# Optimization experiments

Hardware: AMD Instinct MI355X
Metric: run time of the kernel (lower is better)

## Reference

```python
import jax, jax.numpy as jnp
from jax import lax
import numpy as np

S, D, L, H, C = 128, 3, 16, 512, 10
B, T = 32, 16384


def setup_inputs() -> dict:
    key = jax.random.key(0)
    ks = jax.random.split(key, 6)
    x = jax.random.normal(ks[0], (B, D, T), dtype=jnp.float32)
    shapelets = jax.random.normal(ks[1], (S, 1, D, L), dtype=jnp.float32)  # OIHW, one per shapelet
    W1 = jax.random.normal(ks[2], (H, S), dtype=jnp.float32) * (1.0 / np.sqrt(S))
    b1 = jnp.zeros((H,), dtype=jnp.float32)
    W2 = jax.random.normal(ks[3], (C, H), dtype=jnp.float32) * (1.0 / np.sqrt(H))
    b2 = jnp.zeros((C,), dtype=jnp.float32)
    return {"x": x, "shapelets": shapelets, "W1": W1, "b1": b1, "W2": W2, "b2": b2}


def reference(x, shapelets, W1, b1, W2, b2):
    # x: [B, D, T] -> [B, 1, D, T]; kernels slide only over time (full-height conv).
    x4 = x[:, None, :, :]
    dn = ("NCHW", "OIHW", "NCHW")
    ones_k = jnp.ones((1, 1, shapelets.shape[2], shapelets.shape[3]), dtype=x.dtype)
    # ||window||^2 per sliding window: [B, 1, 1, Tout]
    window_square = lax.conv_general_dilated(x4 * x4, ones_k, (1, 1), "VALID", dimension_numbers=dn)
    # all cross-correlations in one grouped conv: [B, S, 1, Tout]
    cross_corr = lax.conv_general_dilated(x4, shapelets, (1, 1), "VALID", dimension_numbers=dn)
    shapelet_square = jnp.sum(shapelets * shapelets, axis=(1, 2, 3))  # [S]
    # squared distance per (shapelet, window), min-reduced over windows
    dist = window_square + shapelet_square[None, :, None, None] - 2.0 * cross_corr  # [B, S, 1, Tout]
    distance = jnp.min(dist, axis=(2, 3))  # [B, S]
    h = jax.nn.relu(distance @ W1.T + b1)
    classification = h @ W2.T + b2
    return (distance, classification)
```

## Files before the change

kernel.cpp:

```cpp
#include <hip/hip_runtime.h>

#define Bn 32
#define Tn 16384
#define Ln 16
#define Sn 128
#define Hn 512
#define Cn 10
#define Kn 48
#define TOUT 16369
#define CH 1024
#define NCH 16
#define XBP 8224
#define NGRP 3168

typedef short  s16x8  __attribute__((ext_vector_type(8)));
typedef float  f32x16 __attribute__((ext_vector_type(16)));

static __device__ __forceinline__ unsigned short f2bf(float f) {
    union { float f; unsigned int u; } v; v.f = f;
    unsigned int r = v.u + 0x7FFF + ((v.u >> 16) & 1);
    return (unsigned short)(r >> 16);
}
static __device__ __forceinline__ unsigned int pk(float a, float b) {
    return (unsigned int)f2bf(a) | ((unsigned int)f2bf(b) << 16);
}
static __device__ __forceinline__ unsigned int pk2(unsigned short a, unsigned short b) {
    return (unsigned int)a | ((unsigned int)b << 16);
}
static __device__ __forceinline__ int swz(int g) { return g ^ ((g >> 3) & 7); }

static __device__ __forceinline__ s16x8 mk_a(unsigned int d0, unsigned int d1,
                                             unsigned int d2, unsigned int d3) {
    union { unsigned int u[4]; s16x8 v; } t;
    t.u[0] = d0; t.u[1] = d1; t.u[2] = d2; t.u[3] = d3;
    return t.v;
}

__global__ __launch_bounds__(256) void prep_kernel(const float* __restrict__ x,
                                                   const float* __restrict__ sh,
                                                   unsigned int* __restrict__ shb,
                                                   float* __restrict__ shsq_g,
                                                   float* __restrict__ wsq_g,
                                                   unsigned int* __restrict__ xg) {
    const int tid = threadIdx.x;
    if (blockIdx.x == 0) {
        if (tid < Sn) {
            const float4* r4 = (const float4*)(sh + tid * Kn);
            float v[48]; float q = 0.f;
            #pragma unroll
            for (int c = 0; c < 12; ++c) {
                const float4 t = r4[c];
                v[4*c] = t.x; v[4*c+1] = t.y; v[4*c+2] = t.z; v[4*c+3] = t.w;
                q = fmaf(t.x, t.x, q); q = fmaf(t.y, t.y, q);
                q = fmaf(t.z, t.z, q); q = fmaf(t.w, t.w, q);
            }
            shsq_g[tid] = q;
            uint4* dst = (uint4*)(shb + tid * 24);
            #pragma unroll
            for (int c = 0; c < 6; ++c) {
                uint4 o;
                o.x = pk(-2.f*v[8*c  ], -2.f*v[8*c+1]);
                o.y = pk(-2.f*v[8*c+2], -2.f*v[8*c+3]);
                o.z = pk(-2.f*v[8*c+4], -2.f*v[8*c+5]);
                o.w = pk(-2.f*v[8*c+6], -2.f*v[8*c+7]);
                dst[c] = o;
            }
        } else {
            const int idx = tid - 128;
            const uint4 z = {0u, 0u, 0u, 0u};
            for (int r = idx; r < 768; r += 128) {
                uint4* d = (uint4*)(xg + r * XBP + 8192);
                #pragma unroll
                for (int q = 0; q < 8; ++q) d[q] = z;
            }
        }
        return;
    }
    const int bid = blockIdx.x - 1;
    const int b  = bid >> 3;
    const int t0 = ((bid & 7) << 11) + 8 * tid;
    float q[8] = {0.f,0.f,0.f,0.f,0.f,0.f,0.f,0.f};
    #pragma unroll
    for (int ch = 0; ch < 3; ++ch) {
        const float* xs = x + (b * 3 + ch) * Tn + t0;
        float wv[24];
        if (t0 + 24 <= Tn) {
            const float4* x4 = (const float4*)xs;
            #pragma unroll
            for (int c = 0; c < 6; ++c) {
                const float4 t = x4[c];
                wv[4*c] = t.x; wv[4*c+1] = t.y; wv[4*c+2] = t.z; wv[4*c+3] = t.w;
            }
        } else {
            #pragma unroll
            for (int k = 0; k < 24; ++k) wv[k] = (t0 + k < Tn) ? xs[k] : 0.f;
        }
        float s = 0.f;
        #pragma unroll
        for (int l = 0; l < 16; ++l) s = fmaf(wv[l], wv[l], s);
        q[0] += s;
        #pragma unroll
        for (int j = 1; j < 8; ++j) {
            s = s - wv[j-1]*wv[j-1] + wv[j+15]*wv[j+15];
            q[j] += s;
        }
        unsigned short bf[24];
        #pragma unroll
        for (int k = 0; k < 24; ++k) bf[k] = f2bf(wv[k]);
        #pragma unroll
        for (int p = 0; p < 8; ++p) {
            uint4 o = { pk2(bf[p  ], bf[p+1]), pk2(bf[p+2], bf[p+3]),
                        pk2(bf[p+4], bf[p+5]), pk2(bf[p+6], bf[p+7]) };
            *(uint4*)(xg + ((b * 8 + p) * 3 + ch) * XBP + (t0 >> 1)) = o;
        }
    }
    float4 o0, o1;
    o0.x = (t0+0 >= TOUT) ? 1e30f : q[0]; o0.y = (t0+1 >= TOUT) ? 1e30f : q[1];
    o0.z = (t0+2 >= TOUT) ? 1e30f : q[2]; o0.w = (t0+3 >= TOUT) ? 1e30f : q[3];
    o1.x = (t0+4 >= TOUT) ? 1e30f : q[4]; o1.y = (t0+5 >= TOUT) ? 1e30f : q[5];
    o1.z = (t0+6 >= TOUT) ? 1e30f : q[6]; o1.w = (t0+7 >= TOUT) ? 1e30f : q[7];
    float4* wd = (float4*)(wsq_g + b * Tn + t0);
    wd[0] = o0; wd[1] = o1;
}

__global__ __launch_bounds__(256, 2) void dist_kernel(const unsigned int* __restrict__ shb,
                                                      const float* __restrict__ shsq_g,
                                                      const float* __restrict__ wsq_g,
                                                      const unsigned int* __restrict__ xg,
                                                      float* __restrict__ partial) {
    __shared__ unsigned int xph[NGRP * 4];
    __shared__ float wsq[16 * 64];
    __shared__ float wavemin[4 * Sn];

    const int tid   = threadIdx.x;
    const int b     = blockIdx.x >> 4;
    const int chunk = blockIdx.x & 15;
    const int tb    = chunk * CH;
    const int lane  = tid & 63;
    const int w     = tid >> 6;
    const int n     = lane & 31;
    const int h     = lane >> 5;

    s16x8 bfr[3][4];
    float shsqv[4];
    #pragma unroll
    for (int st = 0; st < 4; ++st) {
        const uint4* base = (const uint4*)(shb + (st * 32 + n) * 24);
        #pragma unroll
        for (int kk = 0; kk < 3; ++kk) {
            const uint4 t = base[kk * 2 + h];
            bfr[kk][st] = mk_a(t.x, t.y, t.z, t.w);
        }
        shsqv[st] = shsq_g[st * 32 + n];
    }

    {
        const unsigned int* xgb = xg + b * 24 * XBP + (tb >> 1);
        for (int g = tid; g < NGRP; g += 256) {
            const int r = g / 132, c = g - r * 132;
            const uint4 v = *(const uint4*)(xgb + r * XBP + (c << 2));
            *(uint4*)((char*)xph + (swz(g) << 4)) = v;
        }
    }

    {
        const float4 v = *(const float4*)(wsq_g + b * Tn + tb + 4 * tid);
        const int t0 = 4 * tid;
        wsq[((t0    ) & 15) * 64 + ((t0    ) >> 4)] = v.x;
        wsq[((t0 + 1) & 15) * 64 + ((t0 + 1) >> 4)] = v.y;
        wsq[((t0 + 2) & 15) * 64 + ((t0 + 2) >> 4)] = v.z;
        wsq[((t0 + 3) & 15) * 64 + ((t0 + 3) >> 4)] = v.w;
    }
    __syncthreads();

    float mcol[4] = {1e30f, 1e30f, 1e30f, 1e30f};
    const f32x16 zero16 = {0.f, 0.f, 0.f, 0.f, 0.f, 0.f, 0.f, 0.f,
                           0.f, 0.f, 0.f, 0.f, 0.f, 0.f, 0.f, 0.f};
    #pragma unroll 2
    for (int rr = 0; rr < 8; ++rr) {
        const int tau = 8 * w + rr;
        const int i   = (tau & 15) + ((tau >> 4) << 9);
        const int p   = i & 7;
        const int gb  = (i >> 3) + 2 * n + h;
        const int r0  = p * 3 * 132;
        const s16x8 a0 = *(const s16x8*)((const char*)xph + (swz(r0 + gb)       << 4));
        const s16x8 a1 = *(const s16x8*)((const char*)xph + (swz(r0 + 132 + gb) << 4));
        const s16x8 a2 = *(const s16x8*)((const char*)xph + (swz(r0 + 264 + gb) << 4));

        f32x16 acc[4];
        #pragma unroll
        for (int st = 0; st < 4; ++st) {
            acc[st] = __builtin_amdgcn_mfma_f32_32x32x16_bf16(a0, bfr[0][st], zero16, 0, 0, 0);
            acc[st] = __builtin_amdgcn_mfma_f32_32x32x16_bf16(a1, bfr[1][st], acc[st], 0, 0, 0);
            acc[st] = __builtin_amdgcn_mfma_f32_32x32x16_bf16(a2, bfr[2][st], acc[st], 0, 0, 0);
        }

        const int ilow = i & 15, ihi = i >> 9;
        float4 wq[4];
        #pragma unroll
        for (int q = 0; q < 4; ++q)
            wq[q] = *(const float4*)&wsq[ilow * 64 + 8 * q + 4 * h + 32 * ihi];

        #pragma unroll
        for (int st = 0; st < 4; ++st)
            #pragma unroll
            for (int reg = 0; reg < 16; reg += 2) {
                const float u = acc[st][reg]     + ((const float*)&wq[reg >> 2])[(reg & 3)];
                const float v = acc[st][reg + 1] + ((const float*)&wq[reg >> 2])[(reg & 3) + 1];
                mcol[st] = fminf(fminf(mcol[st], u), v);
            }
    }

    #pragma unroll
    for (int st = 0; st < 4; ++st) {
        float mm = mcol[st] + shsqv[st];
        mm = fminf(mm, __shfl_xor(mm, 32, 64));
        if (h == 0) wavemin[w * Sn + st * 32 + n] = mm;
    }
    __syncthreads();
    if (tid < Sn) {
        const float mm = fminf(fminf(wavemin[tid], wavemin[Sn + tid]),
                               fminf(wavemin[2 * Sn + tid], wavemin[3 * Sn + tid]));
        partial[(b * NCH + chunk) * Sn + tid] = mm;
    }
}

__global__ __launch_bounds__(512) void mlp_kernel(const float* __restrict__ partial,
                                                  const float* __restrict__ W1,
                                                  const float* __restrict__ b1,
                                                  const float* __restrict__ W2,
                                                  const float* __restrict__ b2,
                                                  float* __restrict__ out) {
    __shared__ float pmin[4][Sn];
    __shared__ float db[Sn];
    __shared__ float hb[Hn];
    __shared__ float part[Cn][32];
    const int b = blockIdx.x, tid = threadIdx.x;

    {
        const int s = tid & 127, g = tid >> 7;
        const float* pp = partial + (b * NCH + g * 4) * Sn + s;
        float m = pp[0];
        #pragma unroll
        for (int c = 1; c < 4; ++c) m = fminf(m, pp[c * Sn]);
        pmin[g][s] = m;
    }
    __syncthreads();
    if (tid < Sn) {
        const float m = fminf(fminf(pmin[0][tid], pmin[1][tid]),
                              fminf(pmin[2][tid], pmin[3][tid]));
        db[tid] = m;
        out[b * Sn + tid] = m;
    }
    __syncthreads();

    float a = b1[tid];
    const float4* w1r = (const float4*)(W1 + tid * Sn);
    const float4* dbv = (const float4*)db;
    #pragma unroll
    for (int i = 0; i < Sn / 4; ++i) {
        const float4 wv = w1r[i];
        const float4 dv = dbv[i];
        a = fmaf(dv.x, wv.x, a); a = fmaf(dv.y, wv.y, a);
        a = fmaf(dv.z, wv.z, a); a = fmaf(dv.w, wv.w, a);
    }
    hb[tid] = fmaxf(a, 0.0f);
    __syncthreads();

    if (tid < Cn * 32) {
        const int c = tid >> 5, p = tid & 31;
        float acc = 0.f;
        #pragma unroll
        for (int i = 0; i < Hn / 32; ++i)
            acc = fmaf(hb[p + 32 * i], W2[c * Hn + p + 32 * i], acc);
        part[c][p] = acc;
    }
    __syncthreads();
    if (tid < Cn) {
        float acc = b2[tid];
        #pragma unroll
        for (int p = 0; p < 32; ++p) acc += part[tid][p];
        out[Bn * Sn + b * Cn + tid] = acc;
    }
}

extern "C" void kernel_launch(void* const* d_in, const int* in_sizes, int n_in,
                              void* d_out, int out_size, void* d_ws, size_t ws_size,
                              hipStream_t stream) {
    const float* x  = (const float*)d_in[0];
    const float* sh = (const float*)d_in[1];
    const float* W1 = (const float*)d_in[2];
    const float* b1 = (const float*)d_in[3];
    const float* W2 = (const float*)d_in[4];
    const float* b2 = (const float*)d_in[5];
    float* out = (float*)d_out;

    char* wsb = (char*)d_ws;
    float*        partial = (float*)wsb;
    unsigned int* shb     = (unsigned int*)(wsb + 262144);
    float*        shsq_g  = (float*)(wsb + 274432);
    float*        wsq_g   = (float*)(wsb + 278528);
    unsigned int* xg      = (unsigned int*)(wsb + 2375680);

    prep_kernel<<<257, 256, 0, stream>>>(x, sh, shb, shsq_g, wsq_g, xg);
    dist_kernel<<<Bn * NCH, 256, 0, stream>>>(shb, shsq_g, wsq_g, xg, partial);
    mlp_kernel<<<Bn, 512, 0, stream>>>(partial, W1, b1, W2, b2, out);
}
```

Measured before the change: 101.5 us.

## Drop LDS staging in dist kernel, read operands from global, split shapelets across blocks

The distance kernel stops staging the bf16 x-shift tiles and window-square values in shared memory and loads MFMA A-operands and window squares directly from global memory (L2-resident). The prep kernel writes window squares pre-transposed into a [16][1024] layout per batch and uses a finer grid. The distance kernel also splits the 128 shapelets into two halves per block, doubling the grid and raising the occupancy hint to 3. This removes the LDS fill and barrier and raises parallelism, but relies on cache hits for repeated global reads and duplicates x loads across the two shapelet halves.

Measured after the change: 99.74 us. About the same (-1.7%).

```diff
diff --git a/kernel.cpp b/kernel.cpp
--- a/kernel.cpp
+++ b/kernel.cpp
@@ -11,7 +11,6 @@
 #define CH 1024
 #define NCH 16
 #define XBP 8224
-#define NGRP 3168
 
 typedef short  s16x8  __attribute__((ext_vector_type(8)));
 typedef float  f32x16 __attribute__((ext_vector_type(16)));
@@ -27,20 +26,15 @@
 static __device__ __forceinline__ unsigned int pk2(unsigned short a, unsigned short b) {
     return (unsigned int)a | ((unsigned int)b << 16);
 }
-static __device__ __forceinline__ int swz(int g) { return g ^ ((g >> 3) & 7); }
-
-static __device__ __forceinline__ s16x8 mk_a(unsigned int d0, unsigned int d1,
-                                             unsigned int d2, unsigned int d3) {
-    union { unsigned int u[4]; s16x8 v; } t;
-    t.u[0] = d0; t.u[1] = d1; t.u[2] = d2; t.u[3] = d3;
-    return t.v;
+static __device__ __forceinline__ s16x8 mk_a(uint4 t) {
+    union { uint4 u; s16x8 v; } c; c.u = t; return c.v;
 }
 
 __global__ __launch_bounds__(256) void prep_kernel(const float* __restrict__ x,
                                                    const float* __restrict__ sh,
                                                    unsigned int* __restrict__ shb,
                                                    float* __restrict__ shsq_g,
-                                                   float* __restrict__ wsq_g,
+                                                   float* __restrict__ wsqT,
                                                    unsigned int* __restrict__ xg) {
     const int tid = threadIdx.x;
     if (blockIdx.x == 0) {
@@ -77,132 +71,112 @@
         return;
     }
     const int bid = blockIdx.x - 1;
-    const int b  = bid >> 3;
-    const int t0 = ((bid & 7) << 11) + 8 * tid;
-    float q[8] = {0.f,0.f,0.f,0.f,0.f,0.f,0.f,0.f};
+    const int b    = bid >> 4;
+    const int t0   = ((bid & 15) << 10) + 4 * tid;
+    float q[4] = {0.f, 0.f, 0.f, 0.f};
     #pragma unroll
     for (int ch = 0; ch < 3; ++ch) {
         const float* xs = x + (b * 3 + ch) * Tn + t0;
-        float wv[24];
-        if (t0 + 24 <= Tn) {
+        float wv[20];
+        if (t0 + 20 <= Tn) {
             const float4* x4 = (const float4*)xs;
             #pragma unroll
-            for (int c = 0; c < 6; ++c) {
+            for (int c = 0; c < 5; ++c) {
                 const float4 t = x4[c];
                 wv[4*c] = t.x; wv[4*c+1] = t.y; wv[4*c+2] = t.z; wv[4*c+3] = t.w;
             }
         } else {
             #pragma unroll
-            for (int k = 0; k < 24; ++k) wv[k] = (t0 + k < Tn) ? xs[k] : 0.f;
+            for (int k = 0; k < 20; ++k) wv[k] = (t0 + k < Tn) ? xs[k] : 0.f;
         }
         float s = 0.f;
         #pragma unroll
         for (int l = 0; l < 16; ++l) s = fmaf(wv[l], wv[l], s);
         q[0] += s;
         #pragma unroll
-        for (int j = 1; j < 8; ++j) {
+        for (int j = 1; j < 4; ++j) {
             s = s - wv[j-1]*wv[j-1] + wv[j+15]*wv[j+15];
             q[j] += s;
         }
-        unsigned short bf[24];
-        #pragma unroll
-        for (int k = 0; k < 24; ++k) bf[k] = f2bf(wv[k]);
+        unsigned short bf[20];
+        #pragma unroll
+        for (int k = 0; k < 20; ++k) bf[k] = f2bf(wv[k]);
+        unsigned int* xrow = xg + (b * 24 + ch) * XBP + (t0 >> 1);
         #pragma unroll
         for (int p = 0; p < 8; ++p) {
-            uint4 o = { pk2(bf[p  ], bf[p+1]), pk2(bf[p+2], bf[p+3]),
-                        pk2(bf[p+4], bf[p+5]), pk2(bf[p+6], bf[p+7]) };
-            *(uint4*)(xg + ((b * 8 + p) * 3 + ch) * XBP + (t0 >> 1)) = o;
-        }
-    }
-    float4 o0, o1;
-    o0.x = (t0+0 >= TOUT) ? 1e30f : q[0]; o0.y = (t0+1 >= TOUT) ? 1e30f : q[1];
-    o0.z = (t0+2 >= TOUT) ? 1e30f : q[2]; o0.w = (t0+3 >= TOUT) ? 1e30f : q[3];
-    o1.x = (t0+4 >= TOUT) ? 1e30f : q[4]; o1.y = (t0+5 >= TOUT) ? 1e30f : q[5];
-    o1.z = (t0+6 >= TOUT) ? 1e30f : q[6]; o1.w = (t0+7 >= TOUT) ? 1e30f : q[7];
-    float4* wd = (float4*)(wsq_g + b * Tn + t0);
-    wd[0] = o0; wd[1] = o1;
-}
-
-__global__ __launch_bounds__(256, 2) void dist_kernel(const unsigned int* __restrict__ shb,
+            uint2 o = { pk2(bf[p], bf[p+1]), pk2(bf[p+2], bf[p+3]) };
+            *(uint2*)(xrow + p * 3 * XBP) = o;
+        }
+    }
+    const int r0 = t0 & 15, col = t0 >> 4;
+    float* wrow = wsqT + b * (16 * 1024) + col;
+    #pragma unroll
+    for (int c = 0; c < 4; ++c)
+        wrow[(r0 + c) * 1024] = (t0 + c >= TOUT) ? 1e30f : q[c];
+}
+
+__global__ __launch_bounds__(256, 3) void dist_kernel(const unsigned int* __restrict__ shb,
                                                       const float* __restrict__ shsq_g,
-                                                      const float* __restrict__ wsq_g,
+                                                      const float* __restrict__ wsqT,
                                                       const unsigned int* __restrict__ xg,
                                                       float* __restrict__ partial) {
-    __shared__ unsigned int xph[NGRP * 4];
-    __shared__ float wsq[16 * 64];
-    __shared__ float wavemin[4 * Sn];
+    __shared__ float wavemin[4 * 64];
 
     const int tid   = threadIdx.x;
-    const int b     = blockIdx.x >> 4;
-    const int chunk = blockIdx.x & 15;
+    const int b     = blockIdx.x >> 5;
+    const int rem   = blockIdx.x & 31;
+    const int chunk = rem >> 1;
+    const int half  = rem & 1;
     const int tb    = chunk * CH;
     const int lane  = tid & 63;
     const int w     = tid >> 6;
     const int n     = lane & 31;
     const int h     = lane >> 5;
 
-    s16x8 bfr[3][4];
-    float shsqv[4];
-    #pragma unroll
-    for (int st = 0; st < 4; ++st) {
-        const uint4* base = (const uint4*)(shb + (st * 32 + n) * 24);
-        #pragma unroll
-        for (int kk = 0; kk < 3; ++kk) {
-            const uint4 t = base[kk * 2 + h];
-            bfr[kk][st] = mk_a(t.x, t.y, t.z, t.w);
-        }
-        shsqv[st] = shsq_g[st * 32 + n];
-    }
-
-    {
-        const unsigned int* xgb = xg + b * 24 * XBP + (tb >> 1);
-        for (int g = tid; g < NGRP; g += 256) {
-            const int r = g / 132, c = g - r * 132;
-            const uint4 v = *(const uint4*)(xgb + r * XBP + (c << 2));
-            *(uint4*)((char*)xph + (swz(g) << 4)) = v;
-        }
-    }
-
-    {
-        const float4 v = *(const float4*)(wsq_g + b * Tn + tb + 4 * tid);
-        const int t0 = 4 * tid;
-        wsq[((t0    ) & 15) * 64 + ((t0    ) >> 4)] = v.x;
-        wsq[((t0 + 1) & 15) * 64 + ((t0 + 1) >> 4)] = v.y;
-        wsq[((t0 + 2) & 15) * 64 + ((t0 + 2) >> 4)] = v.z;
-        wsq[((t0 + 3) & 15) * 64 + ((t0 + 3) >> 4)] = v.w;
-    }
-    __syncthreads();
-
-    float mcol[4] = {1e30f, 1e30f, 1e30f, 1e30f};
+    s16x8 bfr[3][2];
+    float shsqv[2];
+    #pragma unroll
+    for (int st = 0; st < 2; ++st) {
+        const int s = half * 64 + st * 32 + n;
+        const uint4* base = (const uint4*)(shb + s * 24);
+        #pragma unroll
+        for (int kk = 0; kk < 3; ++kk)
+            bfr[kk][st] = mk_a(base[kk * 2 + h]);
+        shsqv[st] = shsq_g[s];
+    }
+
+    float mcol[2] = {1e30f, 1e30f};
     const f32x16 zero16 = {0.f, 0.f, 0.f, 0.f, 0.f, 0.f, 0.f, 0.f,
                            0.f, 0.f, 0.f, 0.f, 0.f, 0.f, 0.f, 0.f};
+    const unsigned int* xgb  = xg + b * 24 * XBP + (tb >> 1);
+    const float*        wrowb = wsqT + b * (16 * 1024) + (tb >> 4);
+
     #pragma unroll 2
     for (int rr = 0; rr < 8; ++rr) {
         const int tau = 8 * w + rr;
         const int i   = (tau & 15) + ((tau >> 4) << 9);
         const int p   = i & 7;
-        const int gb  = (i >> 3) + 2 * n + h;
-        const int r0  = p * 3 * 132;
-        const s16x8 a0 = *(const s16x8*)((const char*)xph + (swz(r0 + gb)       << 4));
-        const s16x8 a1 = *(const s16x8*)((const char*)xph + (swz(r0 + 132 + gb) << 4));
-        const s16x8 a2 = *(const s16x8*)((const char*)xph + (swz(r0 + 264 + gb) << 4));
-
-        f32x16 acc[4];
-        #pragma unroll
-        for (int st = 0; st < 4; ++st) {
+        const unsigned int* arow = xgb + p * 3 * XBP + (((i & ~7) >> 1) + 8 * n + 4 * h);
+        const s16x8 a0 = mk_a(*(const uint4*)(arow));
+        const s16x8 a1 = mk_a(*(const uint4*)(arow + XBP));
+        const s16x8 a2 = mk_a(*(const uint4*)(arow + 2 * XBP));
+
+        f32x16 acc[2];
+        #pragma unroll
+        for (int st = 0; st < 2; ++st) {
             acc[st] = __builtin_amdgcn_mfma_f32_32x32x16_bf16(a0, bfr[0][st], zero16, 0, 0, 0);
             acc[st] = __builtin_amdgcn_mfma_f32_32x32x16_bf16(a1, bfr[1][st], acc[st], 0, 0, 0);
             acc[st] = __builtin_amdgcn_mfma_f32_32x32x16_bf16(a2, bfr[2][st], acc[st], 0, 0, 0);
         }
 
-        const int ilow = i & 15, ihi = i >> 9;
+        const float* wrow = wrowb + (i & 15) * 1024 + ((i >> 9) << 5);
         float4 wq[4];
         #pragma unroll
         for (int q = 0; q < 4; ++q)
-            wq[q] = *(const float4*)&wsq[ilow * 64 + 8 * q + 4 * h + 32 * ihi];
-
-        #pragma unroll
-        for (int st = 0; st < 4; ++st)
+            wq[q] = *(const float4*)(wrow + 8 * q + 4 * h);
+
+        #pragma unroll
+        for (int st = 0; st < 2; ++st)
             #pragma unroll
             for (int reg = 0; reg < 16; reg += 2) {
                 const float u = acc[st][reg]     + ((const float*)&wq[reg >> 2])[(reg & 3)];
@@ -212,16 +186,16 @@
     }
 
     #pragma unroll
-    for (int st = 0; st < 4; ++st) {
+    for (int st = 0; st < 2; ++st) {
         float mm = mcol[st] + shsqv[st];
         mm = fminf(mm, __shfl_xor(mm, 32, 64));
-        if (h == 0) wavemin[w * Sn + st * 32 + n] = mm;
-    }
-    __syncthreads();
-    if (tid < Sn) {
-        const float mm = fminf(fminf(wavemin[tid], wavemin[Sn + tid]),
-                               fminf(wavemin[2 * Sn + tid], wavemin[3 * Sn + tid]));
-        partial[(b * NCH + chunk) * Sn + tid] = mm;
+        if (h == 0) wavemin[w * 64 + st * 32 + n] = mm;
+    }
+    __syncthreads();
+    if (tid < 64) {
+        const float mm = fminf(fminf(wavemin[tid], wavemin[64 + tid]),
+                               fminf(wavemin[128 + tid], wavemin[192 + tid]));
+        partial[(b * NCH + chunk) * Sn + half * 64 + tid] = mm;
     }
 }
 
@@ -299,10 +273,10 @@
     float*        partial = (float*)wsb;
     unsigned int* shb     = (unsigned int*)(wsb + 262144);
     float*        shsq_g  = (float*)(wsb + 274432);
-    float*        wsq_g   = (float*)(wsb + 278528);
+    float*        wsqT    = (float*)(wsb + 278528);
     unsigned int* xg      = (unsigned int*)(wsb + 2375680);
 
-    prep_kernel<<<257, 256, 0, stream>>>(x, sh, shb, shsq_g, wsq_g, xg);
-    dist_kernel<<<Bn * NCH, 256, 0, stream>>>(shb, shsq_g, wsq_g, xg, partial);
+    prep_kernel<<<513, 256, 0, stream>>>(x, sh, shb, shsq_g, wsqT, xg);
+    dist_kernel<<<Bn * NCH * 2, 256, 0, stream>>>(shb, shsq_g, wsqT, xg, partial);
     mlp_kernel<<<Bn, 512, 0, stream>>>(partial, W1, b1, W2, b2, out);
 }
```
